# Kernel optimization log

Measured on AMD Instinct MI355X. Metric: run time of the kernel, lower is better.

## Reference

```python
import jax, jax.numpy as jnp
import numpy as np

B, D_MODEL, HIDEEN, HEAD, IMG_H, IMG_W = 16, 512, 512, 8, 32, 32
D_K = D_MODEL // HEAD
EPS = 1e-5


def setup_inputs() -> dict:
    key = jax.random.key(0)
    ks = jax.random.split(key, 9)
    s_in = 1.0 / np.sqrt(D_MODEL)
    s_h = 1.0 / np.sqrt(HIDEEN)
    return {
        "x": jax.random.normal(ks[0], (B, D_MODEL, IMG_H, IMG_W), jnp.float32),
        "Wq": jax.random.uniform(ks[1], (HIDEEN, D_MODEL), jnp.float32, -s_in, s_in),
        "bq": jax.random.uniform(ks[2], (HIDEEN,), jnp.float32, -s_in, s_in),
        "Wk": jax.random.uniform(ks[3], (HIDEEN, D_MODEL), jnp.float32, -s_in, s_in),
        "bk": jax.random.uniform(ks[4], (HIDEEN,), jnp.float32, -s_in, s_in),
        "Wv": jax.random.uniform(ks[5], (HIDEEN, D_MODEL), jnp.float32, -s_in, s_in),
        "bv": jax.random.uniform(ks[6], (HIDEEN,), jnp.float32, -s_in, s_in),
        "Wo": jax.random.uniform(ks[7], (HIDEEN, HIDEEN), jnp.float32, -s_h, s_h),
        "bo": jax.random.uniform(ks[8], (HIDEEN,), jnp.float32, -s_h, s_h),
    }


def _conv1x1(x, W, b):
    # x: [B, Cin, H, W], W: [Cout, Cin]
    return jnp.einsum("bchw,oc->bohw", x, W) + b[None, :, None, None]


def _heads(t):
    # torch: [B, C, H, W] -> view(B, -1, head, d_k) -> transpose(1, 2)
    return t.reshape(B, -1, HEAD, D_K).transpose(0, 2, 1, 3)  # [B, head, N, d_k]


def reference(x, Wq, bq, Wk, bk, Wv, bv, Wo, bo):
    q = _heads(_conv1x1(x, Wq, bq))
    k = _heads(_conv1x1(x, Wk, bk))
    v = _heads(_conv1x1(x, Wv, bv))
    scores = jnp.einsum("bhnd,bhmd->bhnm", q, k) / np.sqrt(D_K).astype(np.float32)
    attn = jax.nn.softmax(scores, axis=-1)
    out = jnp.einsum("bhnm,bhmd->bhnd", attn, v)  # [B, head, N, d_k]
    # back to image layout: [B, N, head*d_k] -> [B, hideen, H, W]
    out = out.transpose(0, 2, 1, 3).reshape(B, -1, HEAD * D_K)
    out = out.transpose(0, 2, 1).reshape(B, -1, IMG_H, IMG_W)
    out = _conv1x1(out, Wo, bo)
    # InstanceNorm2d (affine=False, biased var, eps=1e-5)
    mu = out.mean(axis=(2, 3), keepdims=True)
    var = out.var(axis=(2, 3), keepdims=True)
    out = (out - mu) / jnp.sqrt(var + EPS)
    # original applies the SAME attn_out conv a second time
    out = _conv1x1(out, Wo, bo)
    return out
```

## Files before the change

kernel.cpp:

```cpp
#include <hip/hip_runtime.h>


typedef short bf16x8_t __attribute__((ext_vector_type(8)));
typedef float f32x4_t  __attribute__((ext_vector_type(4)));

union U4 {
  uint4 u;
  bf16x8_t v;
  unsigned short us[8];
};

__device__ __forceinline__ unsigned short f2bf(float f) {
  union { float f; unsigned int u; } x; x.f = f;
  unsigned int r = x.u + 0x7fffu + ((x.u >> 16) & 1u);
  return (unsigned short)(r >> 16);
}

#define BATCH_STRIDE (512 * 1024)

__global__ __launch_bounds__(256) void cvtx_k(
    const float* __restrict__ x, unsigned short* __restrict__ xb)
{
  __shared__ float tile[32][33];
  const int b = blockIdx.z, c0 = blockIdx.y * 32, n0 = blockIdx.x * 32;
  const int t = threadIdx.x;
  {
    const int cl_ = t >> 3, n4 = (t & 7) * 4;
    const float4 u = *(const float4*)(x + (size_t)b * BATCH_STRIDE
                                      + (size_t)(c0 + cl_) * 1024 + n0 + n4);
    tile[cl_][n4] = u.x; tile[cl_][n4 + 1] = u.y;
    tile[cl_][n4 + 2] = u.z; tile[cl_][n4 + 3] = u.w;
  }
  __syncthreads();
  {
    const int nl = t >> 3, c4 = (t & 7) * 4;
    ushort4 o;
    o.x = f2bf(tile[c4][nl]);     o.y = f2bf(tile[c4 + 1][nl]);
    o.z = f2bf(tile[c4 + 2][nl]); o.w = f2bf(tile[c4 + 3][nl]);
    *(ushort4*)(xb + (size_t)b * BATCH_STRIDE + (size_t)(n0 + nl) * 512
                + c0 + c4) = o;
  }
}

template<int OUTF>
__device__ __forceinline__ void gemm_core(
    const float* __restrict__ W, const float* __restrict__ bias,
    const unsigned short* __restrict__ src, void* __restrict__ dst,
    int m0, int n0, int b, unsigned short* sA, unsigned short* sB)
{
  const int t = threadIdx.x;
  const int lane = t & 63, wv = t >> 6, qd = lane >> 4, cl = lane & 15;
  const int wm = wv >> 1, wn = wv & 1;
  const unsigned short* srcb = src + (size_t)b * BATCH_STRIDE + (size_t)n0 * 512;

  f32x4_t acc[4][4];
  #pragma unroll
  for (int i = 0; i < 4; ++i)
    #pragma unroll
    for (int f = 0; f < 4; ++f) acc[i][f] = (f32x4_t){0.f, 0.f, 0.f, 0.f};

  const int ar = t >> 2, akf = (t & 3) * 8;

  for (int kk = 0; kk < 512; kk += 32) {
    if (kk) __syncthreads();
    #pragma unroll
    for (int p = 0; p < 2; ++p) {
      const int row = p * 64 + ar;
      const float* wr = W + (size_t)(m0 + row) * 512 + kk + akf;
      const float4 w0 = *(const float4*)wr;
      const float4 w1 = *(const float4*)(wr + 4);
      U4 wa;
      wa.us[0] = f2bf(w0.x); wa.us[1] = f2bf(w0.y);
      wa.us[2] = f2bf(w0.z); wa.us[3] = f2bf(w0.w);
      wa.us[4] = f2bf(w1.x); wa.us[5] = f2bf(w1.y);
      wa.us[6] = f2bf(w1.z); wa.us[7] = f2bf(w1.w);
      *(uint4*)(sA + row * 40 + akf) = wa.u;
      *(uint4*)(sB + row * 40 + akf) =
          *(const uint4*)(srcb + (size_t)row * 512 + kk + akf);
    }
    __syncthreads();
    U4 af[4], bf[4];
    #pragma unroll
    for (int i = 0; i < 4; ++i) {
      af[i].u = *(const uint4*)(sA + (wm * 64 + i * 16 + cl) * 40 + qd * 8);
      bf[i].u = *(const uint4*)(sB + (wn * 64 + i * 16 + cl) * 40 + qd * 8);
    }
    #pragma unroll
    for (int i = 0; i < 4; ++i)
      #pragma unroll
      for (int f = 0; f < 4; ++f)
        acc[i][f] = __builtin_amdgcn_mfma_f32_16x16x32_bf16(
            af[i].v, bf[f].v, acc[i][f], 0, 0, 0);
  }

  #pragma unroll
  for (int i = 0; i < 4; ++i) {
    #pragma unroll
    for (int r = 0; r < 4; ++r) {
      const int o = m0 + wm * 64 + i * 16 + qd * 4 + r;
      const float bv = bias[o];
      #pragma unroll
      for (int f = 0; f < 4; ++f) {
        const int n = n0 + wn * 64 + f * 16 + cl;
        const size_t idx = (size_t)b * BATCH_STRIDE + (size_t)o * 1024 + n;
        const float val = acc[i][f][r] + bv;
        if (OUTF) ((float*)dst)[idx] = val;
        else      ((unsigned short*)dst)[idx] = f2bf(val);
      }
    }
  }
}

struct QKVArgs {
  const float* W[3];
  const float* bias[3];
  unsigned short* dst[3];
};

__global__ __launch_bounds__(256) void qkv_k(
    QKVArgs args, const unsigned short* __restrict__ xb)
{
  __shared__ __align__(16) unsigned short sA[128 * 40];
  __shared__ __align__(16) unsigned short sB[128 * 40];
  const int widx = blockIdx.y >> 2;
  const int m0 = (blockIdx.y & 3) * 128;
  gemm_core<0>(args.W[widx], args.bias[widx], xb, args.dst[widx],
               m0, blockIdx.x * 128, blockIdx.z, sA, sB);
}

template<int OUTF>
__global__ __launch_bounds__(256) void gemm_wo_k(
    const float* __restrict__ W, const float* __restrict__ bias,
    const unsigned short* __restrict__ src, void* __restrict__ dst)
{
  __shared__ __align__(16) unsigned short sA[128 * 40];
  __shared__ __align__(16) unsigned short sB[128 * 40];
  gemm_core<OUTF>(W, bias, src, dst, blockIdx.y * 128, blockIdx.x * 128,
                  blockIdx.z, sA, sB);
}

__global__ __launch_bounds__(256) void attn_k(
    const unsigned short* __restrict__ Q,
    const unsigned short* __restrict__ K,
    const unsigned short* __restrict__ V,
    unsigned short* __restrict__ O)
{
  __shared__ __align__(16) unsigned short sK[64 * 72];
  __shared__ __align__(16) unsigned short sV[64 * 72];
  __shared__ __align__(16) unsigned short sP[4 * 16 * 72];

  const int t = threadIdx.x;
  const int lane = t & 63, wv = t >> 6, qd = lane >> 4, cl = lane & 15;
  const int b = blockIdx.y >> 3, h = blockIdx.y & 7;
  const int i0 = blockIdx.x * 64;
  const size_t bbase = (size_t)b * BATCH_STRIDE;
  const int hoff = h * 64;

  U4 aq0, aq1;
  {
    const unsigned short* qp =
        Q + bbase + (size_t)(i0 + wv * 16 + cl) * 512 + hoff + qd * 8;
    aq0.u = *(const uint4*)qp;
    aq1.u = *(const uint4*)(qp + 32);
  }

  f32x4_t oacc[4];
  #pragma unroll
  for (int f = 0; f < 4; ++f) oacc[f] = (f32x4_t){0.f, 0.f, 0.f, 0.f};
  float rs[4] = {0.f, 0.f, 0.f, 0.f};

  for (int j0 = 0; j0 < 1024; j0 += 64) {
    __syncthreads();
    #pragma unroll
    for (int p = 0; p < 2; ++p) {
      const int ki = p * 32 + (t >> 3), kd0 = (t & 7) * 8;
      *(uint4*)(sK + ki * 72 + kd0) =
          *(const uint4*)(K + bbase + (size_t)(j0 + ki) * 512 + hoff + kd0);
    }
    #pragma unroll
    for (int p = 0; p < 2; ++p) {
      const int vi = t & 63, vd0 = (t >> 6) * 8 + p * 32;
      U4 u; u.u = *(const uint4*)(V + bbase + (size_t)(j0 + vi) * 512 + hoff + vd0);
      #pragma unroll
      for (int j = 0; j < 8; ++j) sV[(vd0 + j) * 72 + vi] = u.us[j];
    }
    __syncthreads();

    f32x4_t s[4];
    #pragma unroll
    for (int nh = 0; nh < 4; ++nh) {
      s[nh] = (f32x4_t){0.f, 0.f, 0.f, 0.f};
      U4 bk0; bk0.u = *(const uint4*)(sK + (nh * 16 + cl) * 72 + qd * 8);
      U4 bk1; bk1.u = *(const uint4*)(sK + (nh * 16 + cl) * 72 + 32 + qd * 8);
      s[nh] = __builtin_amdgcn_mfma_f32_16x16x32_bf16(aq0.v, bk0.v, s[nh], 0, 0, 0);
      s[nh] = __builtin_amdgcn_mfma_f32_16x16x32_bf16(aq1.v, bk1.v, s[nh], 0, 0, 0);
    }

    #pragma unroll
    for (int nh = 0; nh < 4; ++nh) {
      #pragma unroll
      for (int r = 0; r < 4; ++r) {
        const float pv = __expf(s[nh][r] * 0.125f);
        sP[wv * 1152 + (qd * 4 + r) * 72 + nh * 16 + cl] = f2bf(pv);
        rs[r] += pv;
      }
    }

    __syncthreads();

    U4 pf0, pf1;
    pf0.u = *(const uint4*)(sP + wv * 1152 + cl * 72 + qd * 8);
    pf1.u = *(const uint4*)(sP + wv * 1152 + cl * 72 + 32 + qd * 8);
    #pragma unroll
    for (int f = 0; f < 4; ++f) {
      U4 vf0, vf1;
      vf0.u = *(const uint4*)(sV + (f * 16 + cl) * 72 + qd * 8);
      vf1.u = *(const uint4*)(sV + (f * 16 + cl) * 72 + 32 + qd * 8);
      oacc[f] = __builtin_amdgcn_mfma_f32_16x16x32_bf16(pf0.v, vf0.v, oacc[f], 0, 0, 0);
      oacc[f] = __builtin_amdgcn_mfma_f32_16x16x32_bf16(pf1.v, vf1.v, oacc[f], 0, 0, 0);
    }
  }

  #pragma unroll
  for (int m = 1; m < 16; m <<= 1)
    #pragma unroll
    for (int r = 0; r < 4; ++r) rs[r] += __shfl_xor(rs[r], m);

  #pragma unroll
  for (int f = 0; f < 4; ++f) {
    #pragma unroll
    for (int r = 0; r < 4; ++r) {
      const int i = i0 + wv * 16 + qd * 4 + r;
      const int j = hoff + f * 16 + cl;
      O[bbase + (size_t)i * 512 + j] = f2bf(oacc[f][r] / rs[r]);
    }
  }
}

__global__ __launch_bounds__(256) void norm_k(
    const float* __restrict__ x, unsigned short* __restrict__ y)
{
  __shared__ float tile[8][1028];
  __shared__ float shm[8], shv[8];
  const int b = blockIdx.x >> 6, c0 = (blockIdx.x & 63) * 8;
  const int t = threadIdx.x;
  const int ch = t >> 5, ln = t & 31;
  const float* xr = x + (size_t)b * BATCH_STRIDE + (size_t)(c0 + ch) * 1024;
  float s1 = 0.f, s2 = 0.f;
  #pragma unroll
  for (int j = 0; j < 8; ++j) {
    const int n = ln * 4 + j * 128;
    const float4 u = *(const float4*)(xr + n);
    tile[ch][n] = u.x; tile[ch][n + 1] = u.y;
    tile[ch][n + 2] = u.z; tile[ch][n + 3] = u.w;
    s1 += u.x + u.y + u.z + u.w;
    s2 += u.x * u.x + u.y * u.y + u.z * u.z + u.w * u.w;
  }
  #pragma unroll
  for (int m = 1; m < 32; m <<= 1) {
    s1 += __shfl_xor(s1, m);
    s2 += __shfl_xor(s2, m);
  }
  if (ln == 0) {
    const float mean = s1 * (1.f / 1024.f);
    const float var = s2 * (1.f / 1024.f) - mean * mean;
    shm[ch] = mean;
    shv[ch] = rsqrtf(var + 1e-5f);
  }
  __syncthreads();
  unsigned short* yb = y + (size_t)b * BATCH_STRIDE;
  #pragma unroll
  for (int jn = 0; jn < 4; ++jn) {
    const int n = t + jn * 256;
    U4 o;
    #pragma unroll
    for (int c = 0; c < 8; ++c)
      o.us[c] = f2bf((tile[c][n] - shm[c]) * shv[c]);
    *(uint4*)(yb + (size_t)n * 512 + c0) = o.u;
  }
}

extern "C" void kernel_launch(void* const* d_in, const int* in_sizes, int n_in,
                              void* d_out, int out_size, void* d_ws, size_t ws_size,
                              hipStream_t stream) {
  const float* x  = (const float*)d_in[0];
  const float* Wq = (const float*)d_in[1];
  const float* bq = (const float*)d_in[2];
  const float* Wk = (const float*)d_in[3];
  const float* bk = (const float*)d_in[4];
  const float* Wv = (const float*)d_in[5];
  const float* bv = (const float*)d_in[6];
  const float* Wo = (const float*)d_in[7];
  const float* bo = (const float*)d_in[8];

  const size_t BUF = (size_t)16 * BATCH_STRIDE;
  unsigned short* xb = (unsigned short*)d_ws;
  unsigned short* Qb = xb + BUF;
  unsigned short* Kb = Qb + BUF;
  unsigned short* Vb = (unsigned short*)d_out;
  unsigned short* Ob = Vb + BUF;
  float*          out1f = (float*)d_ws;
  unsigned short* out1n = Kb;

  QKVArgs qa;
  qa.W[0] = Wq; qa.W[1] = Wk; qa.W[2] = Wv;
  qa.bias[0] = bq; qa.bias[1] = bk; qa.bias[2] = bv;
  qa.dst[0] = Qb; qa.dst[1] = Kb; qa.dst[2] = Vb;

  cvtx_k<<<dim3(32, 16, 16), 256, 0, stream>>>(x, xb);
  qkv_k<<<dim3(8, 12, 16), 256, 0, stream>>>(qa, xb);
  attn_k<<<dim3(16, 128), 256, 0, stream>>>(Qb, Kb, Vb, Ob);
  gemm_wo_k<1><<<dim3(8, 4, 16), 256, 0, stream>>>(Wo, bo, Ob, out1f);
  norm_k<<<dim3(16 * 64), 256, 0, stream>>>(out1f, out1n);
  gemm_wo_k<1><<<dim3(8, 4, 16), 256, 0, stream>>>(Wo, bo, out1n, d_out);
}
```

Baseline: 292.8 us.

## Pre-transpose V, double attention query tile, use direct global-to-LDS loads in GEMM

Adds a separate kernel that transposes V into a head-dim-major buffer, so attention loads V tiles with vector stores instead of scattered per-element LDS writes. The attention kernel now processes 32 query rows per wave (128 per block), reusing each K/V tile for twice as many queries and halving the grid. The GEMM core loads the activation operand straight into LDS with global_load_lds and drops the row padding, and the float-to-bf16 packing is done in pairs. The cost is an extra kernel launch plus a full V round trip through memory, and the unpadded LDS layout may cause bank conflicts on the fragment reads.

```diff
diff --git a/kernel.cpp b/kernel.cpp
--- a/kernel.cpp
+++ b/kernel.cpp
@@ -4,17 +4,22 @@
 typedef short bf16x8_t __attribute__((ext_vector_type(8)));
 typedef float f32x4_t  __attribute__((ext_vector_type(4)));
 
-union U4 {
-  uint4 u;
-  bf16x8_t v;
-  unsigned short us[8];
-};
+union U4 { uint4 u; bf16x8_t v; unsigned short us[8]; };
 
 __device__ __forceinline__ unsigned short f2bf(float f) {
   union { float f; unsigned int u; } x; x.f = f;
   unsigned int r = x.u + 0x7fffu + ((x.u >> 16) & 1u);
   return (unsigned short)(r >> 16);
 }
+__device__ __forceinline__ unsigned int f2bf2(float lo, float hi) {
+  return (unsigned int)f2bf(lo) | ((unsigned int)f2bf(hi) << 16);
+}
+__device__ __forceinline__ void ld_lds16(const unsigned short* g,
+                                         unsigned short* l) {
+  __builtin_amdgcn_global_load_lds(
+      (const __attribute__((address_space(1))) unsigned int*)g,
+      (__attribute__((address_space(3))) unsigned int*)l, 16, 0, 0);
+}
 
 #define BATCH_STRIDE (512 * 1024)
 
@@ -25,20 +30,20 @@
   const int b = blockIdx.z, c0 = blockIdx.y * 32, n0 = blockIdx.x * 32;
   const int t = threadIdx.x;
   {
-    const int cl_ = t >> 3, n4 = (t & 7) * 4;
+    const int cr = t >> 3, n4 = (t & 7) * 4;
     const float4 u = *(const float4*)(x + (size_t)b * BATCH_STRIDE
-                                      + (size_t)(c0 + cl_) * 1024 + n0 + n4);
-    tile[cl_][n4] = u.x; tile[cl_][n4 + 1] = u.y;
-    tile[cl_][n4 + 2] = u.z; tile[cl_][n4 + 3] = u.w;
+                                      + (size_t)(c0 + cr) * 1024 + n0 + n4);
+    tile[cr][n4] = u.x; tile[cr][n4 + 1] = u.y;
+    tile[cr][n4 + 2] = u.z; tile[cr][n4 + 3] = u.w;
   }
   __syncthreads();
   {
     const int nl = t >> 3, c4 = (t & 7) * 4;
-    ushort4 o;
-    o.x = f2bf(tile[c4][nl]);     o.y = f2bf(tile[c4 + 1][nl]);
-    o.z = f2bf(tile[c4 + 2][nl]); o.w = f2bf(tile[c4 + 3][nl]);
-    *(ushort4*)(xb + (size_t)b * BATCH_STRIDE + (size_t)(n0 + nl) * 512
-                + c0 + c4) = o;
+    uint2 o;
+    o.x = f2bf2(tile[c4][nl], tile[c4 + 1][nl]);
+    o.y = f2bf2(tile[c4 + 2][nl], tile[c4 + 3][nl]);
+    *(uint2*)(xb + (size_t)b * BATCH_STRIDE + (size_t)(n0 + nl) * 512
+              + c0 + c4) = o;
   }
 }
 
@@ -59,38 +64,35 @@
     #pragma unroll
     for (int f = 0; f < 4; ++f) acc[i][f] = (f32x4_t){0.f, 0.f, 0.f, 0.f};
 
-  const int ar = t >> 2, akf = (t & 3) * 8;
+  const int srow = t >> 2, sch = (t & 3) * 8;
 
   for (int kk = 0; kk < 512; kk += 32) {
     if (kk) __syncthreads();
     #pragma unroll
     for (int p = 0; p < 2; ++p) {
-      const int row = p * 64 + ar;
-      const float* wr = W + (size_t)(m0 + row) * 512 + kk + akf;
+      ld_lds16(srcb + (size_t)(p * 64 + srow) * 512 + kk + sch,
+               sB + p * 2048 + t * 8);
+      const float* wr = W + (size_t)(m0 + p * 64 + srow) * 512 + kk + sch;
       const float4 w0 = *(const float4*)wr;
       const float4 w1 = *(const float4*)(wr + 4);
-      U4 wa;
-      wa.us[0] = f2bf(w0.x); wa.us[1] = f2bf(w0.y);
-      wa.us[2] = f2bf(w0.z); wa.us[3] = f2bf(w0.w);
-      wa.us[4] = f2bf(w1.x); wa.us[5] = f2bf(w1.y);
-      wa.us[6] = f2bf(w1.z); wa.us[7] = f2bf(w1.w);
-      *(uint4*)(sA + row * 40 + akf) = wa.u;
-      *(uint4*)(sB + row * 40 + akf) =
-          *(const uint4*)(srcb + (size_t)row * 512 + kk + akf);
+      uint4 wa;
+      wa.x = f2bf2(w0.x, w0.y); wa.y = f2bf2(w0.z, w0.w);
+      wa.z = f2bf2(w1.x, w1.y); wa.w = f2bf2(w1.z, w1.w);
+      *(uint4*)(sA + p * 2048 + t * 8) = wa;
     }
     __syncthreads();
-    U4 af[4], bf[4];
+    U4 af[4], bfr[4];
     #pragma unroll
     for (int i = 0; i < 4; ++i) {
-      af[i].u = *(const uint4*)(sA + (wm * 64 + i * 16 + cl) * 40 + qd * 8);
-      bf[i].u = *(const uint4*)(sB + (wn * 64 + i * 16 + cl) * 40 + qd * 8);
+      af[i].u  = *(const uint4*)(sA + (wm * 64 + i * 16 + cl) * 32 + qd * 8);
+      bfr[i].u = *(const uint4*)(sB + (wn * 64 + i * 16 + cl) * 32 + qd * 8);
     }
     #pragma unroll
     for (int i = 0; i < 4; ++i)
       #pragma unroll
       for (int f = 0; f < 4; ++f)
         acc[i][f] = __builtin_amdgcn_mfma_f32_16x16x32_bf16(
-            af[i].v, bf[f].v, acc[i][f], 0, 0, 0);
+            af[i].v, bfr[f].v, acc[i][f], 0, 0, 0);
   }
 
   #pragma unroll
@@ -120,8 +122,8 @@
 __global__ __launch_bounds__(256) void qkv_k(
     QKVArgs args, const unsigned short* __restrict__ xb)
 {
-  __shared__ __align__(16) unsigned short sA[128 * 40];
-  __shared__ __align__(16) unsigned short sB[128 * 40];
+  __shared__ __align__(16) unsigned short sA[128 * 32];
+  __shared__ __align__(16) unsigned short sB[128 * 32];
   const int widx = blockIdx.y >> 2;
   const int m0 = (blockIdx.y & 3) * 128;
   gemm_core<0>(args.W[widx], args.bias[widx], xb, args.dst[widx],
@@ -133,108 +135,151 @@
     const float* __restrict__ W, const float* __restrict__ bias,
     const unsigned short* __restrict__ src, void* __restrict__ dst)
 {
-  __shared__ __align__(16) unsigned short sA[128 * 40];
-  __shared__ __align__(16) unsigned short sB[128 * 40];
+  __shared__ __align__(16) unsigned short sA[128 * 32];
+  __shared__ __align__(16) unsigned short sB[128 * 32];
   gemm_core<OUTF>(W, bias, src, dst, blockIdx.y * 128, blockIdx.x * 128,
                   blockIdx.z, sA, sB);
+}
+
+__global__ __launch_bounds__(256) void vt_k(
+    const unsigned short* __restrict__ V, unsigned short* __restrict__ Vt)
+{
+  __shared__ unsigned short sT[64 * 72];
+  const int b = blockIdx.z, p0 = blockIdx.x * 64, j0 = blockIdx.y * 64;
+  const int t = threadIdx.x;
+  const int r = t >> 2, c8 = (t & 3) * 8;
+  #pragma unroll
+  for (int p = 0; p < 2; ++p)
+    *(uint4*)(sT + r * 72 + c8 + p * 32) =
+        *(const uint4*)(V + (size_t)b * BATCH_STRIDE
+                        + (size_t)(p0 + r) * 512 + j0 + c8 + p * 32);
+  __syncthreads();
+  #pragma unroll
+  for (int p = 0; p < 2; ++p) {
+    U4 o;
+    #pragma unroll
+    for (int e = 0; e < 8; ++e) o.us[e] = sT[(c8 + p * 32 + e) * 72 + r];
+    *(uint4*)(Vt + (size_t)b * BATCH_STRIDE + (size_t)(j0 + r) * 1024
+              + p0 + c8 + p * 32) = o.u;
+  }
 }
 
 __global__ __launch_bounds__(256) void attn_k(
     const unsigned short* __restrict__ Q,
     const unsigned short* __restrict__ K,
-    const unsigned short* __restrict__ V,
+    const unsigned short* __restrict__ Vt,
     unsigned short* __restrict__ O)
 {
-  __shared__ __align__(16) unsigned short sK[64 * 72];
-  __shared__ __align__(16) unsigned short sV[64 * 72];
-  __shared__ __align__(16) unsigned short sP[4 * 16 * 72];
+  __shared__ __align__(16) unsigned short sK[64 * 80];
+  __shared__ __align__(16) unsigned short sV[64 * 80];
+  __shared__ __align__(16) unsigned short sP[4 * 32 * 80];
 
   const int t = threadIdx.x;
   const int lane = t & 63, wv = t >> 6, qd = lane >> 4, cl = lane & 15;
   const int b = blockIdx.y >> 3, h = blockIdx.y & 7;
-  const int i0 = blockIdx.x * 64;
+  const int i0 = blockIdx.x * 128;
   const size_t bbase = (size_t)b * BATCH_STRIDE;
   const int hoff = h * 64;
-
-  U4 aq0, aq1;
-  {
+  unsigned short* sPw = sP + wv * 2560;
+
+  U4 aq[2][2];
+  #pragma unroll
+  for (int mt = 0; mt < 2; ++mt) {
     const unsigned short* qp =
-        Q + bbase + (size_t)(i0 + wv * 16 + cl) * 512 + hoff + qd * 8;
-    aq0.u = *(const uint4*)qp;
-    aq1.u = *(const uint4*)(qp + 32);
-  }
-
-  f32x4_t oacc[4];
-  #pragma unroll
-  for (int f = 0; f < 4; ++f) oacc[f] = (f32x4_t){0.f, 0.f, 0.f, 0.f};
-  float rs[4] = {0.f, 0.f, 0.f, 0.f};
+        Q + bbase + (size_t)(i0 + wv * 32 + mt * 16 + cl) * 512 + hoff;
+    aq[mt][0].u = *(const uint4*)(qp + qd * 8);
+    aq[mt][1].u = *(const uint4*)(qp + 32 + qd * 8);
+  }
+
+  f32x4_t oacc[2][4];
+  #pragma unroll
+  for (int mt = 0; mt < 2; ++mt)
+    #pragma unroll
+    for (int f = 0; f < 4; ++f) oacc[mt][f] = (f32x4_t){0.f, 0.f, 0.f, 0.f};
+  float rs[2][4] = {{0.f, 0.f, 0.f, 0.f}, {0.f, 0.f, 0.f, 0.f}};
+
+  const int srow = t >> 2, sch = (t & 3) * 8;
 
   for (int j0 = 0; j0 < 1024; j0 += 64) {
     __syncthreads();
     #pragma unroll
     for (int p = 0; p < 2; ++p) {
-      const int ki = p * 32 + (t >> 3), kd0 = (t & 7) * 8;
-      *(uint4*)(sK + ki * 72 + kd0) =
-          *(const uint4*)(K + bbase + (size_t)(j0 + ki) * 512 + hoff + kd0);
-    }
-    #pragma unroll
-    for (int p = 0; p < 2; ++p) {
-      const int vi = t & 63, vd0 = (t >> 6) * 8 + p * 32;
-      U4 u; u.u = *(const uint4*)(V + bbase + (size_t)(j0 + vi) * 512 + hoff + vd0);
-      #pragma unroll
-      for (int j = 0; j < 8; ++j) sV[(vd0 + j) * 72 + vi] = u.us[j];
+      *(uint4*)(sK + srow * 80 + sch + p * 32) =
+          *(const uint4*)(K + bbase + (size_t)(j0 + srow) * 512
+                          + hoff + sch + p * 32);
+      *(uint4*)(sV + srow * 80 + sch + p * 32) =
+          *(const uint4*)(Vt + bbase + (size_t)(hoff + srow) * 1024
+                          + j0 + sch + p * 32);
     }
     __syncthreads();
 
-    f32x4_t s[4];
+    f32x4_t s[2][4];
     #pragma unroll
     for (int nh = 0; nh < 4; ++nh) {
-      s[nh] = (f32x4_t){0.f, 0.f, 0.f, 0.f};
-      U4 bk0; bk0.u = *(const uint4*)(sK + (nh * 16 + cl) * 72 + qd * 8);
-      U4 bk1; bk1.u = *(const uint4*)(sK + (nh * 16 + cl) * 72 + 32 + qd * 8);
-      s[nh] = __builtin_amdgcn_mfma_f32_16x16x32_bf16(aq0.v, bk0.v, s[nh], 0, 0, 0);
-      s[nh] = __builtin_amdgcn_mfma_f32_16x16x32_bf16(aq1.v, bk1.v, s[nh], 0, 0, 0);
-    }
-
-    #pragma unroll
-    for (int nh = 0; nh < 4; ++nh) {
-      #pragma unroll
-      for (int r = 0; r < 4; ++r) {
-        const float pv = __expf(s[nh][r] * 0.125f);
-        sP[wv * 1152 + (qd * 4 + r) * 72 + nh * 16 + cl] = f2bf(pv);
-        rs[r] += pv;
+      U4 bk0, bk1;
+      bk0.u = *(const uint4*)(sK + (nh * 16 + cl) * 80 + qd * 8);
+      bk1.u = *(const uint4*)(sK + (nh * 16 + cl) * 80 + 32 + qd * 8);
+      #pragma unroll
+      for (int mt = 0; mt < 2; ++mt) {
+        s[mt][nh] = (f32x4_t){0.f, 0.f, 0.f, 0.f};
+        s[mt][nh] = __builtin_amdgcn_mfma_f32_16x16x32_bf16(
+            aq[mt][0].v, bk0.v, s[mt][nh], 0, 0, 0);
+        s[mt][nh] = __builtin_amdgcn_mfma_f32_16x16x32_bf16(
+            aq[mt][1].v, bk1.v, s[mt][nh], 0, 0, 0);
       }
     }
 
+    #pragma unroll
+    for (int mt = 0; mt < 2; ++mt)
+      #pragma unroll
+      for (int nh = 0; nh < 4; ++nh)
+        #pragma unroll
+        for (int r = 0; r < 4; ++r) {
+          const float pv = __expf(s[mt][nh][r] * 0.125f);
+          sPw[(mt * 16 + qd * 4 + r) * 80 + nh * 16 + cl] = f2bf(pv);
+          rs[mt][r] += pv;
+        }
+
     __syncthreads();
 
-    U4 pf0, pf1;
-    pf0.u = *(const uint4*)(sP + wv * 1152 + cl * 72 + qd * 8);
-    pf1.u = *(const uint4*)(sP + wv * 1152 + cl * 72 + 32 + qd * 8);
+    U4 pf[2][2];
+    #pragma unroll
+    for (int mt = 0; mt < 2; ++mt) {
+      pf[mt][0].u = *(const uint4*)(sPw + (mt * 16 + cl) * 80 + qd * 8);
+      pf[mt][1].u = *(const uint4*)(sPw + (mt * 16 + cl) * 80 + 32 + qd * 8);
+    }
     #pragma unroll
     for (int f = 0; f < 4; ++f) {
       U4 vf0, vf1;
-      vf0.u = *(const uint4*)(sV + (f * 16 + cl) * 72 + qd * 8);
-      vf1.u = *(const uint4*)(sV + (f * 16 + cl) * 72 + 32 + qd * 8);
-      oacc[f] = __builtin_amdgcn_mfma_f32_16x16x32_bf16(pf0.v, vf0.v, oacc[f], 0, 0, 0);
-      oacc[f] = __builtin_amdgcn_mfma_f32_16x16x32_bf16(pf1.v, vf1.v, oacc[f], 0, 0, 0);
+      vf0.u = *(const uint4*)(sV + (f * 16 + cl) * 80 + qd * 8);
+      vf1.u = *(const uint4*)(sV + (f * 16 + cl) * 80 + 32 + qd * 8);
+      #pragma unroll
+      for (int mt = 0; mt < 2; ++mt) {
+        oacc[mt][f] = __builtin_amdgcn_mfma_f32_16x16x32_bf16(
+            pf[mt][0].v, vf0.v, oacc[mt][f], 0, 0, 0);
+        oacc[mt][f] = __builtin_amdgcn_mfma_f32_16x16x32_bf16(
+            pf[mt][1].v, vf1.v, oacc[mt][f], 0, 0, 0);
+      }
     }
   }
 
   #pragma unroll
   for (int m = 1; m < 16; m <<= 1)
     #pragma unroll
-    for (int r = 0; r < 4; ++r) rs[r] += __shfl_xor(rs[r], m);
-
-  #pragma unroll
-  for (int f = 0; f < 4; ++f) {
-    #pragma unroll
-    for (int r = 0; r < 4; ++r) {
-      const int i = i0 + wv * 16 + qd * 4 + r;
-      const int j = hoff + f * 16 + cl;
-      O[bbase + (size_t)i * 512 + j] = f2bf(oacc[f][r] / rs[r]);
-    }
-  }
+    for (int mt = 0; mt < 2; ++mt)
+      #pragma unroll
+      for (int r = 0; r < 4; ++r) rs[mt][r] += __shfl_xor(rs[mt][r], m);
+
+  #pragma unroll
+  for (int mt = 0; mt < 2; ++mt)
+    #pragma unroll
+    for (int f = 0; f < 4; ++f)
+      #pragma unroll
+      for (int r = 0; r < 4; ++r) {
+        const int i = i0 + wv * 32 + mt * 16 + qd * 4 + r;
+        const int j = hoff + f * 16 + cl;
+        O[bbase + (size_t)i * 512 + j] = f2bf(oacc[mt][f][r] / rs[mt][r]);
+      }
 }
 
 __global__ __launch_bounds__(256) void norm_k(
@@ -272,11 +317,12 @@
   #pragma unroll
   for (int jn = 0; jn < 4; ++jn) {
     const int n = t + jn * 256;
-    U4 o;
-    #pragma unroll
-    for (int c = 0; c < 8; ++c)
-      o.us[c] = f2bf((tile[c][n] - shm[c]) * shv[c]);
-    *(uint4*)(yb + (size_t)n * 512 + c0) = o.u;
+    uint4 o;
+    o.x = f2bf2((tile[0][n] - shm[0]) * shv[0], (tile[1][n] - shm[1]) * shv[1]);
+    o.y = f2bf2((tile[2][n] - shm[2]) * shv[2], (tile[3][n] - shm[3]) * shv[3]);
+    o.z = f2bf2((tile[4][n] - shm[4]) * shv[4], (tile[5][n] - shm[5]) * shv[5]);
+    o.w = f2bf2((tile[6][n] - shm[6]) * shv[6], (tile[7][n] - shm[7]) * shv[7]);
+    *(uint4*)(yb + (size_t)n * 512 + c0) = o;
   }
 }
 
@@ -299,6 +345,7 @@
   unsigned short* Kb = Qb + BUF;
   unsigned short* Vb = (unsigned short*)d_out;
   unsigned short* Ob = Vb + BUF;
+  unsigned short* Vt = xb;
   float*          out1f = (float*)d_ws;
   unsigned short* out1n = Kb;
 
@@ -309,7 +356,8 @@
 
   cvtx_k<<<dim3(32, 16, 16), 256, 0, stream>>>(x, xb);
   qkv_k<<<dim3(8, 12, 16), 256, 0, stream>>>(qa, xb);
-  attn_k<<<dim3(16, 128), 256, 0, stream>>>(Qb, Kb, Vb, Ob);
+  vt_k<<<dim3(16, 8, 16), 256, 0, stream>>>(Vb, Vt);
+  attn_k<<<dim3(8, 128), 256, 0, stream>>>(Qb, Kb, Vt, Ob);
   gemm_wo_k<1><<<dim3(8, 4, 16), 256, 0, stream>>>(Wo, bo, Ob, out1f);
   norm_k<<<dim3(16 * 64), 256, 0, stream>>>(out1f, out1n);
   gemm_wo_k<1><<<dim3(8, 4, 16), 256, 0, stream>>>(Wo, bo, out1n, d_out);
```

Result: no change. 298.2 us (+1.8%).
